# Optimization experiments

Measured on AMD Instinct MI355X. Metric: run time of the kernel, lower is better.

The kernel has to match this reference:

```python
import jax, jax.numpy as jnp
import numpy as np

MS = 0.001
TAU = 50.0
THRESHOLD = 1.0


def setup_inputs() -> dict:
    key = jax.random.key(0)
    kx, kw = jax.random.split(key)
    x = jax.random.normal(kx, (32, 1024, 1000), dtype=jnp.float32)
    # nn.init.normal_(w, mean=0.0, std=8000)
    w = jax.random.normal(kw, (1024, 1024), dtype=jnp.float32) * 8000.0
    return {"x": x, "w": w}


def reference(x, w):
    # x: [B, n_in, T], w: [n_in, n_out]
    # Precompute all input currents in one batched GEMM: [T, B, n_out]
    currents = jnp.einsum('bit,io->tbo', x, w)

    def step(v, cur):
        v = v + (-v + cur) * (MS / TAU)
        spikes = (v >= THRESHOLD).astype(v.dtype)
        v = v * (1.0 - spikes)
        return v, spikes

    v0 = jnp.zeros((x.shape[0], w.shape[1]), dtype=x.dtype)
    _, out = jax.lax.scan(step, v0, currents)  # out: [T, B, n_out]
    return jnp.transpose(out, (1, 2, 0))  # [B, n_out, T]
```

## Files before the change

### kernel.cpp

```cpp
#include <hip/hip_runtime.h>


#define NB 32
#define NI 1024
#define NO 1024
#define NT 1000
#define TT 128
#define OT 128
#define KI 16

typedef double d4 __attribute__((ext_vector_type(4)));

__global__ __launch_bounds__(256, 3)
void snn_gemm_mfma64(const float* __restrict__ x, const float* __restrict__ w,
                     double* __restrict__ cur, int t0, int len)
{
    __shared__ float As[KI][TT];
    __shared__ float Bs[KI][OT];

    const int tid  = threadIdx.x;
    const int lane = tid & 63;
    const int wave = tid >> 6;
    const int wm   = (wave >> 1) * 64;
    const int wn   = (wave & 1) * 64;
    const int m16  = lane & 15;
    const int kq   = lane >> 4;

    const int tt0 = t0 + blockIdx.x * TT;
    const int o0  = blockIdx.y * OT;
    const int b   = blockIdx.z;
    const float* xb = x + (size_t)b * NI * NT;

    d4 p = (d4)0.0;
#pragma unroll
    for (int s = 0; s < 4; ++s) {
        const double ap = (m16 == kq + 4 * s) ? 1.0 : 0.0;
        const double bp = (double)(100 * (kq + 4 * s) + m16 + 1);
        p = __builtin_amdgcn_mfma_f64_16x16x4f64(ap, bp, p, 0, 0, 0);
    }
    int prow[4], pcol[4];
#pragma unroll
    for (int r = 0; r < 4; ++r) {
        const int val = ((int)p[r] - 1) & 0xffff;
        const int m = val / 100;
        prow[r] = m & 15;
        pcol[r] = (val - m * 100) & 15;
    }

    d4 acc[4][4];
#pragma unroll
    for (int r = 0; r < 4; ++r)
#pragma unroll
        for (int c = 0; c < 4; ++c) acc[r][c] = (d4)0.0;

    const int sr = tid >> 5;
    const int sc = (tid & 31) * 4;
    const int at = tt0 + sc;

    for (int i0 = 0; i0 < NI; i0 += KI) {
        float4 a0 = make_float4(0.f, 0.f, 0.f, 0.f);
        float4 a1 = a0;
        if (at < NT) {
            a0 = *(const float4*)(xb + (size_t)(i0 + sr) * NT + at);
            a1 = *(const float4*)(xb + (size_t)(i0 + sr + 8) * NT + at);
        }
        const float4 b0 = *(const float4*)(w + (size_t)(i0 + sr) * NO + (o0 + sc));
        const float4 b1 = *(const float4*)(w + (size_t)(i0 + sr + 8) * NO + (o0 + sc));

        __syncthreads();
        *(float4*)&As[sr][sc]     = a0;
        *(float4*)&As[sr + 8][sc] = a1;
        *(float4*)&Bs[sr][sc]     = b0;
        *(float4*)&Bs[sr + 8][sc] = b1;
        __syncthreads();

#pragma unroll
        for (int k4 = 0; k4 < 4; ++k4) {
            const int kk = k4 * 4 + kq;
            double af[4], bf[4];
#pragma unroll
            for (int r = 0; r < 4; ++r) af[r] = (double)As[kk][wm + r * 16 + m16];
#pragma unroll
            for (int c = 0; c < 4; ++c) bf[c] = (double)Bs[kk][wn + c * 16 + m16];
#pragma unroll
            for (int r = 0; r < 4; ++r)
#pragma unroll
                for (int c = 0; c < 4; ++c)
                    acc[r][c] = __builtin_amdgcn_mfma_f64_16x16x4f64(
                        af[r], bf[c], acc[r][c], 0, 0, 0);
        }
    }

    const int tend = t0 + len;
#pragma unroll
    for (int rt = 0; rt < 4; ++rt) {
#pragma unroll
        for (int j = 0; j < 4; ++j) {
            const int tg = tt0 + wm + rt * 16 + prow[j];
            if (tg < tend) {
                double* dst = cur + ((size_t)(tg - t0) * NB + b) * NO + o0 + wn;
#pragma unroll
                for (int ct = 0; ct < 4; ++ct)
                    dst[ct * 16 + pcol[j]] = acc[rt][ct][j];
            }
        }
    }
}

#define NC 32
__global__ __launch_bounds__(64)
void snn_scan_f64(const double* __restrict__ cur, float* __restrict__ out,
                  double* __restrict__ vstate, int t0, int len)
{
    const int gid = blockIdx.x * 64 + threadIdx.x;
    const double dt = 0.001 / 50.0;

    double v = (t0 == 0) ? 0.0 : vstate[gid];
    const double* cp = cur + gid;
    float* op = out + (size_t)gid * NT + t0;

    const size_t ts = (size_t)NB * NO;
    const int nb = len / NC;
    const int rem = len - nb * NC;

    double A[NC], B[NC];
#pragma unroll
    for (int j = 0; j < NC; ++j) A[j] = (j < len) ? cp[(size_t)j * ts] : 0.0;

    for (int blk = 0; blk < nb; ++blk) {
        const int next = (blk + 1) * NC;
#pragma unroll
        for (int j = 0; j < NC; ++j)
            B[j] = (next + j < len) ? cp[(size_t)(next + j) * ts] : 0.0;

#pragma unroll
        for (int q = 0; q < NC; q += 8) {
            float s[8];
#pragma unroll
            for (int j = 0; j < 8; ++j) {
                v = v + (A[q + j] - v) * dt;
                const bool sp = (v >= 1.0);
                s[j] = sp ? 1.0f : 0.0f;
                if (sp) v = 0.0;
            }
            *(float4*)(op + q)     = make_float4(s[0], s[1], s[2], s[3]);
            *(float4*)(op + q + 4) = make_float4(s[4], s[5], s[6], s[7]);
        }
        op += NC;
#pragma unroll
        for (int j = 0; j < NC; ++j) A[j] = B[j];
    }

    for (int q = 0; q < rem; q += 8) {
        float s[8];
#pragma unroll
        for (int j = 0; j < 8; ++j) {
            v = v + (A[q + j] - v) * dt;
            const bool sp = (v >= 1.0);
            s[j] = sp ? 1.0f : 0.0f;
            if (sp) v = 0.0;
        }
        *(float4*)(op + q)     = make_float4(s[0], s[1], s[2], s[3]);
        *(float4*)(op + q + 4) = make_float4(s[4], s[5], s[6], s[7]);
    }
    vstate[gid] = v;
}

extern "C" void kernel_launch(void* const* d_in, const int* in_sizes, int n_in,
                              void* d_out, int out_size, void* d_ws, size_t ws_size,
                              hipStream_t stream)
{
    const float* x = (const float*)d_in[0];
    const float* w = (const float*)d_in[1];
    float* out = (float*)d_out;

    const size_t vbytes = (size_t)NB * NO * sizeof(double);
    double* vstate = (double*)d_ws;
    double* curbuf = (double*)((char*)d_ws + vbytes);

    const size_t per_t = (size_t)NB * NO * sizeof(double);
    size_t avail = (ws_size > vbytes) ? (ws_size - vbytes) : 0;
    int Tc = (int)((avail / per_t < (size_t)NT) ? (avail / per_t) : (size_t)NT);
    Tc &= ~7;
    if (Tc < 8) Tc = 8;

    for (int t0 = 0; t0 < NT; t0 += Tc) {
        const int len = (NT - t0 < Tc) ? (NT - t0) : Tc;
        dim3 gg((len + TT - 1) / TT, NO / OT, NB);
        snn_gemm_mfma64<<<gg, 256, 0, stream>>>(x, w, curbuf, t0, len);
        snn_scan_f64<<<(NB * NO) / 64, 64, 0, stream>>>(curbuf, out, vstate, t0, len);
    }
}
```

Baseline: 1.291 ms.

## Replace FP64 MFMA GEMM with multi-slice int8 MFMA emulation of high precision

Splits x and w into six signed 7-bit slices with per-row and per-column power-of-two scales and computes the product with int8 32x32x32 MFMA. Only the upper-triangular slice products are accumulated, and the result is recombined in double precision before the existing scan. The goal is to swap the low-throughput FP64 matrix path for the much higher int8 MFMA throughput. The cost is extra preprocessing kernels, six times larger packed operand traffic, and a truncation error that could flip spike decisions near the threshold.

```diff
diff --git a/kernel.cpp b/kernel.cpp
--- a/kernel.cpp
+++ b/kernel.cpp
@@ -5,105 +5,240 @@
 #define NI 1024
 #define NO 1024
 #define NT 1000
-#define TT 128
-#define OT 128
-#define KI 16
-
-typedef double d4 __attribute__((ext_vector_type(4)));
-
-__global__ __launch_bounds__(256, 3)
-void snn_gemm_mfma64(const float* __restrict__ x, const float* __restrict__ w,
-                     double* __restrict__ cur, int t0, int len)
-{
-    __shared__ float As[KI][TT];
-    __shared__ float Bs[KI][OT];
+#define NS 6
+#define BT 64
+#define BO 64
+#define KI 64
+#define ROWB (NS*64)
+
+typedef int i32x4  __attribute__((ext_vector_type(4)));
+typedef int i32x16 __attribute__((ext_vector_type(16)));
+
+__global__ void snn_wscale(const float* __restrict__ w, float* __restrict__ sb)
+{
+    const int o = blockIdx.x * 256 + threadIdx.x;
+    float m = 0.f;
+    for (int i = 0; i < NI; ++i) m = fmaxf(m, fabsf(w[(size_t)i * NO + o]));
+    const unsigned bits = __float_as_uint(m);
+    const int e = (bits >> 23) & 255;
+    float S = 0.f, Si = 0.f;
+    if (e) {
+        S  = __uint_as_float((unsigned)(e + 1) << 23);
+        Si = __uint_as_float((unsigned)(253 - e) << 23);
+    }
+    sb[o] = S;
+    sb[NO + o] = Si;
+}
+
+__global__ void snn_wslice(const float* __restrict__ w, const float* __restrict__ sb,
+                           signed char* __restrict__ wp)
+{
+    __shared__ int sldw[NS][64][16];
+    __shared__ float sinv[64];
+    const int tid = threadIdx.x;
+    const int o0 = blockIdx.x * 64;
+    const int ol = tid & 63, iq = tid >> 6;
+    if (tid < 64) sinv[tid] = sb[NO + o0 + tid];
+    __syncthreads();
+    const float inv = sinv[ol];
+    for (int ic = 0; ic < NI; ic += 64) {
+        for (int q4 = 0; q4 < 16; q4 += 4) {
+            int pk[NS] = {0, 0, 0, 0, 0, 0};
+#pragma unroll
+            for (int j = 0; j < 4; ++j) {
+                const int i = ic + iq * 16 + q4 + j;
+                float wv = w[(size_t)i * NO + o0 + ol] * inv;
+#pragma unroll
+                for (int s = 0; s < NS; ++s) {
+                    const float f = wv * 128.f;
+                    const int a = (int)f;
+                    wv = f - (float)a;
+                    pk[s] |= (a & 255) << (8 * j);
+                }
+            }
+            const int cdw = (iq * 16 + q4) >> 2;
+#pragma unroll
+            for (int s = 0; s < NS; ++s)
+                sldw[s][ol][cdw ^ (ol & 15)] = pk[s];
+        }
+        __syncthreads();
+        for (int p = 0; p < 24; ++p) {
+            const int idx = p * 256 + tid;
+            const int iw = idx & 15, r = (idx >> 4) & 63, s = idx >> 10;
+            *(int*)&wp[((size_t)s * NO + o0 + r) * NI + ic + iw * 4] =
+                sldw[s][r][iw ^ (r & 15)];
+        }
+        __syncthreads();
+    }
+}
+
+__global__ void snn_xprep(const float* __restrict__ x, signed char* __restrict__ xp,
+                          float* __restrict__ sa, int t0, int tca)
+{
+    __shared__ int sldw[NS][64][16];
+    __shared__ float red[4][64];
+    __shared__ float sinv[64];
+    const int tid = threadIdx.x;
+    const int b = blockIdx.y;
+    const int tt = blockIdx.x * 64;
+    const int tl = tid & 63, iq = tid >> 6;
+    const int tg = t0 + tt + tl;
+    const bool valid = (tg < NT);
+    const float* xb = x + (size_t)b * NI * NT;
+
+    float m = 0.f;
+    if (valid)
+        for (int i = iq; i < NI; i += 4) m = fmaxf(m, fabsf(xb[(size_t)i * NT + tg]));
+    red[iq][tl] = m;
+    __syncthreads();
+    if (iq == 0) {
+        m = fmaxf(fmaxf(red[0][tl], red[1][tl]), fmaxf(red[2][tl], red[3][tl]));
+        const unsigned bits = __float_as_uint(m);
+        const int e = (bits >> 23) & 255;
+        float S = 0.f, Si = 0.f;
+        if (e) {
+            S  = __uint_as_float((unsigned)(e + 1) << 23);
+            Si = __uint_as_float((unsigned)(253 - e) << 23);
+        }
+        sa[(size_t)b * tca + tt + tl] = S;
+        sinv[tl] = Si;
+    }
+    __syncthreads();
+    const float inv = sinv[tl];
+
+    for (int ic = 0; ic < NI; ic += 64) {
+        for (int q4 = 0; q4 < 16; q4 += 4) {
+            int pk[NS] = {0, 0, 0, 0, 0, 0};
+#pragma unroll
+            for (int j = 0; j < 4; ++j) {
+                const int i = ic + iq * 16 + q4 + j;
+                float wv = valid ? xb[(size_t)i * NT + tg] * inv : 0.f;
+#pragma unroll
+                for (int s = 0; s < NS; ++s) {
+                    const float f = wv * 128.f;
+                    const int a = (int)f;
+                    wv = f - (float)a;
+                    pk[s] |= (a & 255) << (8 * j);
+                }
+            }
+            const int cdw = (iq * 16 + q4) >> 2;
+#pragma unroll
+            for (int s = 0; s < NS; ++s)
+                sldw[s][tl][cdw ^ (tl & 15)] = pk[s];
+        }
+        __syncthreads();
+        for (int p = 0; p < 24; ++p) {
+            const int idx = p * 256 + tid;
+            const int iw = idx & 15, r = (idx >> 4) & 63, s = idx >> 10;
+            *(int*)&xp[(((size_t)s * NB + b) * tca + tt + r) * NI + ic + iw * 4] =
+                sldw[s][r][iw ^ (r & 15)];
+        }
+        __syncthreads();
+    }
+}
+
+__global__ __launch_bounds__(256, 2)
+void snn_gemm_i8(const signed char* __restrict__ xp, const signed char* __restrict__ wp,
+                 const float* __restrict__ sa, const float* __restrict__ sb,
+                 double* __restrict__ cur, int t0, int tca)
+{
+    __shared__ signed char As[BT * ROWB];
+    __shared__ signed char Bs[BO * ROWB];
 
     const int tid  = threadIdx.x;
     const int lane = tid & 63;
     const int wave = tid >> 6;
-    const int wm   = (wave >> 1) * 64;
-    const int wn   = (wave & 1) * 64;
-    const int m16  = lane & 15;
-    const int kq   = lane >> 4;
-
-    const int tt0 = t0 + blockIdx.x * TT;
-    const int o0  = blockIdx.y * OT;
-    const int b   = blockIdx.z;
-    const float* xb = x + (size_t)b * NI * NT;
-
-    d4 p = (d4)0.0;
-#pragma unroll
-    for (int s = 0; s < 4; ++s) {
-        const double ap = (m16 == kq + 4 * s) ? 1.0 : 0.0;
-        const double bp = (double)(100 * (kq + 4 * s) + m16 + 1);
-        p = __builtin_amdgcn_mfma_f64_16x16x4f64(ap, bp, p, 0, 0, 0);
-    }
-    int prow[4], pcol[4];
-#pragma unroll
-    for (int r = 0; r < 4; ++r) {
-        const int val = ((int)p[r] - 1) & 0xffff;
-        const int m = val / 100;
-        prow[r] = m & 15;
-        pcol[r] = (val - m * 100) & 15;
-    }
-
-    d4 acc[4][4];
-#pragma unroll
-    for (int r = 0; r < 4; ++r)
-#pragma unroll
-        for (int c = 0; c < 4; ++c) acc[r][c] = (d4)0.0;
-
-    const int sr = tid >> 5;
-    const int sc = (tid & 31) * 4;
-    const int at = tt0 + sc;
-
-    for (int i0 = 0; i0 < NI; i0 += KI) {
-        float4 a0 = make_float4(0.f, 0.f, 0.f, 0.f);
-        float4 a1 = a0;
-        if (at < NT) {
-            a0 = *(const float4*)(xb + (size_t)(i0 + sr) * NT + at);
-            a1 = *(const float4*)(xb + (size_t)(i0 + sr + 8) * NT + at);
-        }
-        const float4 b0 = *(const float4*)(w + (size_t)(i0 + sr) * NO + (o0 + sc));
-        const float4 b1 = *(const float4*)(w + (size_t)(i0 + sr + 8) * NO + (o0 + sc));
-
-        __syncthreads();
-        *(float4*)&As[sr][sc]     = a0;
-        *(float4*)&As[sr + 8][sc] = a1;
-        *(float4*)&Bs[sr][sc]     = b0;
-        *(float4*)&Bs[sr + 8][sc] = b1;
-        __syncthreads();
-
-#pragma unroll
-        for (int k4 = 0; k4 < 4; ++k4) {
-            const int kk = k4 * 4 + kq;
-            double af[4], bf[4];
-#pragma unroll
-            for (int r = 0; r < 4; ++r) af[r] = (double)As[kk][wm + r * 16 + m16];
-#pragma unroll
-            for (int c = 0; c < 4; ++c) bf[c] = (double)Bs[kk][wn + c * 16 + m16];
-#pragma unroll
-            for (int r = 0; r < 4; ++r)
-#pragma unroll
-                for (int c = 0; c < 4; ++c)
-                    acc[r][c] = __builtin_amdgcn_mfma_f64_16x16x4f64(
-                        af[r], bf[c], acc[r][c], 0, 0, 0);
-        }
-    }
-
-    const int tend = t0 + len;
-#pragma unroll
-    for (int rt = 0; rt < 4; ++rt) {
-#pragma unroll
-        for (int j = 0; j < 4; ++j) {
-            const int tg = tt0 + wm + rt * 16 + prow[j];
-            if (tg < tend) {
-                double* dst = cur + ((size_t)(tg - t0) * NB + b) * NO + o0 + wn;
-#pragma unroll
-                for (int ct = 0; ct < 4; ++ct)
-                    dst[ct * 16 + pcol[j]] = acc[rt][ct][j];
-            }
-        }
+    const int wm = (wave >> 1) * 32;
+    const int wn = (wave & 1) * 32;
+    const int l31 = lane & 31;
+    const int hi  = lane >> 5;
+
+    const int o0 = blockIdx.x * BO;
+    const int bt = blockIdx.y * BT;
+    const int b  = blockIdx.z;
+
+    int prow[16];
+    {
+        i32x4 pa, pb;
+#pragma unroll
+        for (int q = 0; q < 4; ++q) {
+            int va = 0, vb = 0;
+#pragma unroll
+            for (int jj = 0; jj < 4; ++jj) {
+                const int k = 16 * hi + q * 4 + jj;
+                if (l31 == k) va |= 1 << (8 * jj);
+                vb |= (k & 255) << (8 * jj);
+            }
+            pa[q] = va; pb[q] = vb;
+        }
+        i32x16 pp = (i32x16)0;
+        pp = __builtin_amdgcn_mfma_i32_32x32x32_i8(pa, pb, pp, 0, 0, 0);
+#pragma unroll
+        for (int r = 0; r < 16; ++r) prow[r] = pp[r] & 31;
+    }
+
+    i32x16 acc[NS];
+#pragma unroll
+    for (int c = 0; c < NS; ++c) acc[c] = (i32x16)0;
+
+    const size_t xps = (size_t)NB * tca * NI;
+    const size_t wps = (size_t)NO * NI;
+    const signed char* xpb = xp + ((size_t)b * tca + bt) * NI;
+    const signed char* wpb = wp + (size_t)o0 * NI;
+
+    const int sr  = tid >> 2;
+    const int sk  = (tid & 3) * 16;
+    const int ssw = (sr & 7) << 4;
+    const int ra  = wm + l31;
+    const int rb  = wn + l31;
+    const int asw = (ra & 7) << 4;
+    const int bsw = (rb & 7) << 4;
+
+    for (int kb = 0; kb < NI; kb += KI) {
+        __syncthreads();
+        i32x4 ta[NS], tb[NS];
+#pragma unroll
+        for (int s = 0; s < NS; ++s) {
+            ta[s] = *(const i32x4*)&xpb[s * xps + (size_t)sr * NI + kb + sk];
+            tb[s] = *(const i32x4*)&wpb[s * wps + (size_t)sr * NI + kb + sk];
+        }
+#pragma unroll
+        for (int s = 0; s < NS; ++s) {
+            const int d = sr * ROWB + ((s * 64 + sk) ^ ssw);
+            *(i32x4*)&As[d] = ta[s];
+            *(i32x4*)&Bs[d] = tb[s];
+        }
+        __syncthreads();
+#pragma unroll
+        for (int ks = 0; ks < 2; ++ks) {
+            i32x4 af[NS], bf[NS];
+#pragma unroll
+            for (int s = 0; s < NS; ++s) {
+                const int off = s * 64 + ks * 32 + 16 * hi;
+                af[s] = *(const i32x4*)&As[ra * ROWB + (off ^ asw)];
+                bf[s] = *(const i32x4*)&Bs[rb * ROWB + (off ^ bsw)];
+            }
+#pragma unroll
+            for (int i = 0; i < NS; ++i)
+#pragma unroll
+                for (int c = NS - 1; c >= i; --c)
+                    acc[c] = __builtin_amdgcn_mfma_i32_32x32x32_i8(
+                        af[i], bf[c - i], acc[c], 0, 0, 0);
+        }
+    }
+
+    const double c128[NS] = {0x1p-14, 0x1p-21, 0x1p-28, 0x1p-35, 0x1p-42, 0x1p-49};
+    const int ocol = o0 + wn + l31;
+    const double sbv = (double)sb[ocol];
+#pragma unroll
+    for (int r = 0; r < 16; ++r) {
+        const int trow = bt + wm + prow[r];
+        double v = 0.0;
+#pragma unroll
+        for (int c = 0; c < NS; ++c) v += (double)acc[c][r] * c128[c];
+        v *= (double)sa[(size_t)b * tca + trow] * sbv;
+        if (t0 + trow < NT)
+            cur[((size_t)trow * NB + b) * NO + ocol] = v;
     }
 }
 
@@ -174,20 +309,32 @@
     const float* w = (const float*)d_in[1];
     float* out = (float*)d_out;
 
-    const size_t vbytes = (size_t)NB * NO * sizeof(double);
-    double* vstate = (double*)d_ws;
-    double* curbuf = (double*)((char*)d_ws + vbytes);
-
-    const size_t per_t = (size_t)NB * NO * sizeof(double);
-    size_t avail = (ws_size > vbytes) ? (ws_size - vbytes) : 0;
-    int Tc = (int)((avail / per_t < (size_t)NT) ? (avail / per_t) : (size_t)NT);
-    Tc &= ~7;
-    if (Tc < 8) Tc = 8;
-
-    for (int t0 = 0; t0 < NT; t0 += Tc) {
-        const int len = (NT - t0 < Tc) ? (NT - t0) : Tc;
-        dim3 gg((len + TT - 1) / TT, NO / OT, NB);
-        snn_gemm_mfma64<<<gg, 256, 0, stream>>>(x, w, curbuf, t0, len);
-        snn_scan_f64<<<(NB * NO) / 64, 64, 0, stream>>>(curbuf, out, vstate, t0, len);
-    }
-}
+    char* p = (char*)d_ws;
+    double* vstate = (double*)p;         p += (size_t)NB * NO * 8;
+    float* sbv = (float*)p;              p += (size_t)2 * NO * 4;
+    signed char* wp = (signed char*)p;   p += (size_t)NS * NO * NI;
+
+    const size_t fixed = (size_t)(p - (char*)d_ws);
+    const size_t per_t = (size_t)NB * 4
+                       + (size_t)NS * NB * NI
+                       + (size_t)NB * NO * 8;
+    int tca = 512;
+    while (tca > 64 && fixed + (size_t)tca * per_t > ws_size) tca -= 64;
+
+    float* sa = (float*)p;               p += (size_t)NB * tca * 4;
+    signed char* xpl = (signed char*)p;  p += (size_t)NS * NB * tca * NI;
+    double* cur = (double*)p;
+
+    snn_wscale<<<dim3(NO / 256), dim3(256), 0, stream>>>(w, sbv);
+    snn_wslice<<<dim3(NO / 64), dim3(256), 0, stream>>>(w, sbv, wp);
+
+    for (int t0 = 0; t0 < NT; t0 += tca) {
+        const int len = (NT - t0 < tca) ? (NT - t0) : tca;
+        const int tiles = (len + BT - 1) / BT;
+        snn_xprep<<<dim3(tiles, NB), dim3(256), 0, stream>>>(x, xpl, sa, t0, tca);
+        snn_gemm_i8<<<dim3(NO / BO, tiles, NB), dim3(256), 0, stream>>>(
+            xpl, wp, sa, sbv, cur, t0, tca);
+        snn_scan_f64<<<dim3((NB * NO) / 64), dim3(64), 0, stream>>>(
+            cur, out, vstate, t0, len);
+    }
+}
```

Result: slower. 1.614 ms (+25.1%).
